# Optimization experiments

Hardware: AMD Instinct MI355X
Metric: run time of the kernel (lower is better)

## Reference

```python
import jax, jax.numpy as jnp
import numpy as np

B, N, D = 2, 128, 512  # batch, tokens, embed_dim (= in_features = out_features)
LAYERS = 3


def setup_inputs() -> dict:
    key = jax.random.key(0)
    ks = jax.random.split(key, 9)
    s = lambda fan_in: 1.0 / np.sqrt(fan_in)
    return {
        "text_embedding": jax.random.normal(ks[0], (B, N, D), dtype=jnp.float32),
        # weights stored as [in, out] so y = x @ W + b (matches torch Linear math)
        "W_rel": jax.random.uniform(ks[1], (2 * D, D), jnp.float32, -s(2 * D), s(2 * D)),
        "b_rel": jax.random.uniform(ks[2], (D,), jnp.float32, -s(2 * D), s(2 * D)),
        "W_go": jax.random.uniform(ks[3], (D, D), jnp.float32, -s(D), s(D)),
        "b_go": jax.random.uniform(ks[4], (D,), jnp.float32, -s(D), s(D)),
        "W_gr": jax.random.uniform(ks[5], (3 * D, D), jnp.float32, -s(3 * D), s(3 * D)),
        "b_gr": jax.random.uniform(ks[6], (D,), jnp.float32, -s(3 * D), s(3 * D)),
        "W_esa": jax.random.uniform(ks[7], (D, D), jnp.float32, -s(D), s(D)),
        "b_esa": jax.random.uniform(ks[8], (D,), jnp.float32, -s(D), s(D)),
    }


def reference(text_embedding, W_rel, b_rel, W_go, b_go, W_gr, b_gr, W_esa, b_esa):
    x = text_embedding  # [B, N, D]
    n = x.shape[1]
    rel = None
    for i in range(LAYERS):
        new_x = jnp.tanh(x @ W_go + b_go)  # [B, N, D]
        # pairwise broadcast-concat: [B, N, N, 2D]
        a = jnp.broadcast_to(x[:, :, None, :], (x.shape[0], n, n, x.shape[-1]))
        b = jnp.broadcast_to(x[:, None, :, :], (x.shape[0], n, n, x.shape[-1]))
        rlf = jnp.concatenate([a, b], axis=3)
        if i == 0:
            rel = rlf @ W_rel + b_rel  # [B, N, N, D]
        rlf2 = jnp.concatenate([rlf, rel], axis=3)  # [B, N, N, 3D]
        rel = jnp.tanh(rlf2 @ W_gr + b_gr)  # [B, N, N, D]
        x = new_x
    rel = rel @ W_esa + b_esa  # [B, N, N, D]
    # original subtracts max over dim=1 then applies Softmax(dim=1); equivalent to stable softmax over axis 1
    attn = jax.nn.softmax(rel, axis=1)
    rel_out = jnp.sum(attn * rel, axis=-2)  # sum over second N axis -> [B, N, D]
    return (x, rel_out)
```

## Files before the change

### kernel.cpp

```cpp
#include <hip/hip_runtime.h>
#include <hip/hip_bf16.h>
#include <stdint.h>


#define DEV static __device__ __forceinline__

typedef float  f32x4  __attribute__((ext_vector_type(4)));
typedef __bf16 bf16x8 __attribute__((ext_vector_type(8)));

DEV float tanh_fast(float x) {
  float e = __expf(2.0f * x);
  return 1.0f - __fdividef(2.0f, e + 1.0f);
}

DEV void gl_lds16(const void* g, void* l) {
  __builtin_amdgcn_global_load_lds(
      (const __attribute__((address_space(1))) unsigned int*)g,
      (__attribute__((address_space(3))) unsigned int*)l, 16, 0, 0);
}

__global__ __launch_bounds__(256) void wconv_kernel(
    const float* __restrict__ Wc, const float* __restrict__ We,
    __bf16* __restrict__ Wct, __bf16* __restrict__ Wet) {
  const float* W = blockIdx.y ? We : Wc;
  __bf16* Wt = blockIdx.y ? Wet : Wct;
  __shared__ float tile[32][33];
  int t = threadIdx.x;
  int tx = t & 31, ty = t >> 5;
  int bx = blockIdx.x & 15, by = blockIdx.x >> 4;
  int k0 = by * 32, n0 = bx * 32;
#pragma unroll
  for (int r = 0; r < 4; ++r) {
    int k = ty + r * 8;
    tile[k][tx] = W[(size_t)(k0 + k) * 512 + n0 + tx];
  }
  __syncthreads();
#pragma unroll
  for (int r = 0; r < 4; ++r) {
    int n = ty + r * 8;
    Wt[(size_t)(n0 + n) * 512 + k0 + tx] = (__bf16)tile[tx][n];
  }
}

struct SOp {
  const float* X;
  const float* W;
  const float* bias;
  const float* add;
  float* out;
  int M;
  int act;
};
struct SBatch { SOp op[6]; };

__global__ __launch_bounds__(256) void small_gemm_kernel(SBatch batch) {
  const SOp o = batch.op[blockIdx.y];
  const int r0 = (int)(blockIdx.x >> 3) * 16;
  const int c0 = (int)(blockIdx.x & 7) * 64;
  if (r0 >= o.M) return;
  __shared__ float Xs[16][40];
  __shared__ float Ws[32][64];
  const int t = threadIdx.x;
  const int tr = t >> 4;
  const int tc = (t & 15) * 4;
  float a0 = 0.f, a1 = 0.f, a2 = 0.f, a3 = 0.f;
  for (int k0 = 0; k0 < 512; k0 += 32) {
    __syncthreads();
    if (t < 128) {
      int row = t >> 3, col = (t & 7) * 4;
      float4 v = make_float4(0.f, 0.f, 0.f, 0.f);
      if (r0 + row < o.M) v = *(const float4*)&o.X[(size_t)(r0 + row) * 512 + k0 + col];
      *(float4*)&Xs[row][col] = v;
    }
    {
      int row = t >> 3, col = (t & 7) * 8;
      const float4* src = (const float4*)&o.W[(size_t)(k0 + row) * 512 + c0 + col];
      *(float4*)&Ws[row][col]     = src[0];
      *(float4*)&Ws[row][col + 4] = src[1];
    }
    __syncthreads();
#pragma unroll
    for (int k = 0; k < 32; ++k) {
      float a = Xs[tr][k];
      float4 w = *(float4*)&Ws[k][tc];
      a0 += a * w.x; a1 += a * w.y; a2 += a * w.z; a3 += a * w.w;
    }
  }
  const int row = r0 + tr;
  if (row >= o.M) return;
  float4 v = make_float4(a0, a1, a2, a3);
  if (o.bias) {
    float4 bv = *(const float4*)&o.bias[c0 + tc];
    v.x += bv.x; v.y += bv.y; v.z += bv.z; v.w += bv.w;
  }
  if (o.add) {
    float4 av = *(const float4*)&o.add[(size_t)row * 512 + c0 + tc];
    v.x += av.x; v.y += av.y; v.z += av.z; v.w += av.w;
  }
  if (o.act) { v.x = tanh_fast(v.x); v.y = tanh_fast(v.y); v.z = tanh_fast(v.z); v.w = tanh_fast(v.w); }
  *(float4*)&o.out[(size_t)row * 512 + c0 + tc] = v;
}

constexpr int BM = 128, BN = 128, BK = 64;

template <int MODE>
__global__ __launch_bounds__(256, 2) void big_gemm_kernel(
    const __bf16* __restrict__ Ab, const float* __restrict__ Av,
    const float* __restrict__ Cv, const __bf16* __restrict__ Wt,
    const float* __restrict__ P, const float* __restrict__ Q,
    const float* __restrict__ bias, __bf16* __restrict__ outb,
    float* __restrict__ outf) {
  __shared__ __bf16 As[BM * BK];
  __shared__ __bf16 Bs[BN * BK];
  const int t = threadIdx.x;
  const int lane = t & 63;
  const int wave = t >> 6;
  const int bm = (int)blockIdx.x >> 2;
  const int n0 = ((int)blockIdx.x & 3) * BN;
  const size_t r0 = (size_t)bm * BM;
  const int b = bm >> 7;
  const int i = bm & 127;
  const int waveM = wave >> 1, waveN = wave & 1;

  f32x4 vzero = {0.f, 0.f, 0.f, 0.f};
  f32x4 acc[4][4];
#pragma unroll
  for (int a = 0; a < 4; ++a)
#pragma unroll
    for (int c = 0; c < 4; ++c) acc[a][c] = vzero;

  const int jj = t >> 3;
  const int kc = (t & 7) * 8;

  for (int k0 = 0; k0 < 512; k0 += BK) {
    __syncthreads();
    if (MODE == 0) {
      float av[8];
      const float* ap = &Av[((size_t)(b * 128 + i)) * 512 + k0 + kc];
      *(float4*)&av[0] = *(const float4*)ap;
      *(float4*)&av[4] = *(const float4*)(ap + 4);
#pragma unroll
      for (int rnd = 0; rnd < 4; ++rnd) {
        int j = rnd * 32 + jj;
        const float* cp = &Cv[((size_t)(b * 128 + j)) * 512 + k0 + kc];
        float cv[8];
        *(float4*)&cv[0] = *(const float4*)cp;
        *(float4*)&cv[4] = *(const float4*)(cp + 4);
        bf16x8 o;
#pragma unroll
        for (int e = 0; e < 8; ++e) o[e] = (__bf16)tanh_fast(av[e] + cv[e]);
        *(bf16x8*)&As[j * BK + kc] = o;
      }
    } else {
#pragma unroll
      for (int p2 = 0; p2 < 4; ++p2) {
        int rowg = wave * 32 + p2 * 8;
        const __bf16* g = Ab + (r0 + rowg + (lane >> 3)) * 512 + k0 + (lane & 7) * 8;
        gl_lds16(g, &As[rowg * BK]);
      }
    }
#pragma unroll
    for (int p2 = 0; p2 < 4; ++p2) {
      int rowg = wave * 32 + p2 * 8;
      const __bf16* g = Wt + (size_t)(n0 + rowg + (lane >> 3)) * 512 + k0 + (lane & 7) * 8;
      gl_lds16(g, &Bs[rowg * BK]);
    }
    __syncthreads();
#pragma unroll
    for (int kk = 0; kk < 2; ++kk) {
      const int koff = kk * 32 + (lane >> 4) * 8;
      const int ml = lane & 15;
      bf16x8 af[4], bfr[4];
#pragma unroll
      for (int tm = 0; tm < 4; ++tm)
        af[tm] = *(const bf16x8*)&As[(waveM * 64 + tm * 16 + ml) * BK + koff];
#pragma unroll
      for (int tn = 0; tn < 4; ++tn)
        bfr[tn] = *(const bf16x8*)&Bs[(waveN * 64 + tn * 16 + ml) * BK + koff];
#pragma unroll
      for (int tm = 0; tm < 4; ++tm)
#pragma unroll
        for (int tn = 0; tn < 4; ++tn)
          acc[tm][tn] = __builtin_amdgcn_mfma_f32_16x16x32_bf16(af[tm], bfr[tn], acc[tm][tn], 0, 0, 0);
    }
  }

  const int quad = lane >> 4, cl = lane & 15;
#pragma unroll
  for (int tm = 0; tm < 4; ++tm) {
#pragma unroll
    for (int r = 0; r < 4; ++r) {
      const int row = waveM * 64 + tm * 16 + quad * 4 + r;
      const size_t grow = r0 + row;
#pragma unroll
      for (int tn = 0; tn < 4; ++tn) {
        const int col = n0 + waveN * 64 + tn * 16 + cl;
        float v = acc[tm][tn][r];
        if (MODE == 2) {
          v += bias[col];
          outf[grow * 512 + col] = v;
        } else {
          v += P[((size_t)(b * 128 + i)) * 512 + col] +
               Q[((size_t)(b * 128 + row)) * 512 + col];
          outb[grow * 512 + col] = (__bf16)tanh_fast(v);
        }
      }
    }
  }
}

__global__ __launch_bounds__(256) void softmax_ml_kernel(
    const float* __restrict__ S, float* __restrict__ Mb, float* __restrict__ Lb) {
  int idx = blockIdx.x * 256 + threadIdx.x;
  int d = idx & 511;
  int j = (idx >> 9) & 127;
  int b = idx >> 16;
  const float* p = S + ((size_t)b * 16384 + j) * 512 + d;
  float m = -3.4e38f, l = 0.f;
  for (int ii = 0; ii < 128; ++ii) {
    float s = p[(size_t)ii * 65536];
    float nm = fmaxf(m, s);
    l = l * __expf(m - nm) + __expf(s - nm);
    m = nm;
  }
  Mb[idx] = m;
  Lb[idx] = 1.0f / l;
}

__global__ __launch_bounds__(256) void softmax_out_kernel(
    const float* __restrict__ S, const float* __restrict__ Mb,
    const float* __restrict__ Lb, float* __restrict__ outp) {
  int idx = blockIdx.x * 256 + threadIdx.x;
  int d = idx & 511;
  int i = (idx >> 9) & 127;
  int b = idx >> 16;
  const float* sp = S + ((size_t)(b * 128 + i)) * 65536 + d;
  const float* mp = Mb + (size_t)b * 65536 + d;
  const float* lp = Lb + (size_t)b * 65536 + d;
  float acc = 0.f;
  for (int jj = 0; jj < 128; ++jj) {
    float s = sp[(size_t)jj * 512];
    float w = __expf(s - mp[(size_t)jj * 512]) * lp[(size_t)jj * 512];
    acc += w * s;
  }
  outp[idx] = acc;
}

extern "C" void kernel_launch(void* const* d_in, const int* in_sizes, int n_in,
                              void* d_out, int out_size, void* d_ws, size_t ws_size,
                              hipStream_t stream) {
  const float* x0    = (const float*)d_in[0];
  const float* W_rel = (const float*)d_in[1];
  const float* b_rel = (const float*)d_in[2];
  const float* W_go  = (const float*)d_in[3];
  const float* b_go  = (const float*)d_in[4];
  const float* W_gr  = (const float*)d_in[5];
  const float* b_gr  = (const float*)d_in[6];
  const float* W_esa = (const float*)d_in[7];
  const float* b_esa = (const float*)d_in[8];

  const float* Wrel_top = W_rel;
  const float* Wrel_bot = W_rel + 512 * 512;
  const float* Wgr_a = W_gr;
  const float* Wgr_b = W_gr + 512 * 512;
  const float* Wgr_c = W_gr + 2 * 512 * 512;

  char* ws = (char*)d_ws;
  size_t off = 0;
  auto alloc = [&](size_t bytes) -> void* {
    void* p = ws + off;
    off += (bytes + 255) & ~(size_t)255;
    return p;
  };
  const size_t NREL = 16777216ull;
  float*  S     = (float*)alloc(NREL * 4);
  __bf16* relA  = (__bf16*)alloc(NREL * 2);
  __bf16* relB  = (__bf16*)alloc(NREL * 2);
  float* x1  = (float*)alloc(131072 * 4);
  float* x2  = (float*)alloc(131072 * 4);
  float* u0  = (float*)alloc(131072 * 4);
  float* v0  = (float*)alloc(131072 * 4);
  float* p0t = (float*)alloc(131072 * 4);
  float* q0t = (float*)alloc(131072 * 4);
  float* Abuf = (float*)alloc(131072 * 4);
  float* Cbuf = (float*)alloc(131072 * 4);
  float* p1  = (float*)alloc(131072 * 4);
  float* q1  = (float*)alloc(131072 * 4);
  float* p2  = (float*)alloc(131072 * 4);
  float* q2  = (float*)alloc(131072 * 4);
  float* dvec = (float*)alloc(512 * 4);
  float* Mb  = (float*)alloc(131072 * 4);
  float* Lb  = (float*)alloc(131072 * 4);
  __bf16* Wg3t  = (__bf16*)alloc(262144 * 2);
  __bf16* Wesat = (__bf16*)alloc(262144 * 2);

  float* x3out  = (float*)d_out;
  float* relout = (float*)d_out + 131072;

  wconv_kernel<<<dim3(256, 2), 256, 0, stream>>>(Wgr_c, W_esa, Wg3t, Wesat);

  SBatch b1 = {};
  b1.op[0] = {x0, W_go, b_go, nullptr, x1, 256, 1};
  b1.op[1] = {x0, Wrel_top, nullptr, nullptr, u0, 256, 0};
  b1.op[2] = {x0, Wrel_bot, nullptr, nullptr, v0, 256, 0};
  b1.op[3] = {x0, Wgr_a, nullptr, nullptr, p0t, 256, 0};
  b1.op[4] = {x0, Wgr_b, nullptr, nullptr, q0t, 256, 0};
  b1.op[5] = {b_rel, Wgr_c, b_gr, nullptr, dvec, 1, 0};
  small_gemm_kernel<<<dim3(128, 6), 256, 0, stream>>>(b1);

  SBatch b2 = {};
  b2.op[0] = {x1, W_go, b_go, nullptr, x2, 256, 1};
  b2.op[1] = {u0, Wgr_c, dvec, p0t, Abuf, 256, 0};
  b2.op[2] = {v0, Wgr_c, nullptr, q0t, Cbuf, 256, 0};
  b2.op[3] = {x1, Wgr_a, b_gr, nullptr, p1, 256, 0};
  b2.op[4] = {x1, Wgr_b, nullptr, nullptr, q1, 256, 0};
  small_gemm_kernel<<<dim3(128, 5), 256, 0, stream>>>(b2);

  SBatch b3 = {};
  b3.op[0] = {x2, W_go, b_go, nullptr, x3out, 256, 1};
  b3.op[1] = {x2, Wgr_a, b_gr, nullptr, p2, 256, 0};
  b3.op[2] = {x2, Wgr_b, nullptr, nullptr, q2, 256, 0};
  small_gemm_kernel<<<dim3(128, 3), 256, 0, stream>>>(b3);

  big_gemm_kernel<0><<<1024, 256, 0, stream>>>(nullptr, Abuf, Cbuf, Wg3t, p1, q1,
                                               nullptr, relA, nullptr);
  big_gemm_kernel<1><<<1024, 256, 0, stream>>>(relA, nullptr, nullptr, Wg3t, p2, q2,
                                               nullptr, relB, nullptr);
  big_gemm_kernel<2><<<1024, 256, 0, stream>>>(relB, nullptr, nullptr, Wesat, nullptr,
                                               nullptr, b_esa, nullptr, S);

  softmax_ml_kernel<<<512, 256, 0, stream>>>(S, Mb, Lb);
  softmax_out_kernel<<<512, 256, 0, stream>>>(S, Mb, Lb, relout);
}
```

Before: 283.5 us.

## Move small GEMMs to split-bf16 MFMA and materialize first rel layer separately

The small fp32 SIMT GEMMs are replaced with an MFMA kernel that uses a hi/lo bf16 split (three MFMAs per tile) to keep near-fp32 accuracy. Weights and activations are pre-split into hi/lo bf16 buffers, and dvec gets its own tiny kernel. The tanh(A+C) expansion that fed the first big GEMM now runs in a separate elementwise kernel that writes a 32MB bf16 buffer, so every big GEMM can use the direct global-to-LDS load path. This adds extra launches and an extra full-tensor write and read of the first rel layer in exchange for faster small GEMMs.

```diff
diff --git a/kernel.cpp b/kernel.cpp
--- a/kernel.cpp
+++ b/kernel.cpp
@@ -7,6 +7,7 @@
 
 typedef float  f32x4  __attribute__((ext_vector_type(4)));
 typedef __bf16 bf16x8 __attribute__((ext_vector_type(8)));
+typedef __bf16 bf16x4 __attribute__((ext_vector_type(4)));
 
 DEV float tanh_fast(float x) {
   float e = __expf(2.0f * x);
@@ -19,11 +20,11 @@
       (__attribute__((address_space(3))) unsigned int*)l, 16, 0, 0);
 }
 
-__global__ __launch_bounds__(256) void wconv_kernel(
-    const float* __restrict__ Wc, const float* __restrict__ We,
-    __bf16* __restrict__ Wct, __bf16* __restrict__ Wet) {
-  const float* W = blockIdx.y ? We : Wc;
-  __bf16* Wt = blockIdx.y ? Wet : Wct;
+struct WC { const float* W; __bf16* Wh; __bf16* Wl; };
+struct WCBatch { WC w[7]; };
+
+__global__ __launch_bounds__(256) void wconv_kernel(WCBatch wb) {
+  const WC wc = wb.w[blockIdx.y];
   __shared__ float tile[32][33];
   int t = threadIdx.x;
   int tx = t & 31, ty = t >> 5;
@@ -32,81 +33,169 @@
 #pragma unroll
   for (int r = 0; r < 4; ++r) {
     int k = ty + r * 8;
-    tile[k][tx] = W[(size_t)(k0 + k) * 512 + n0 + tx];
+    tile[k][tx] = wc.W[(size_t)(k0 + k) * 512 + n0 + tx];
   }
   __syncthreads();
 #pragma unroll
   for (int r = 0; r < 4; ++r) {
     int n = ty + r * 8;
-    Wt[(size_t)(n0 + n) * 512 + k0 + tx] = (__bf16)tile[tx][n];
-  }
-}
-
-struct SOp {
-  const float* X;
-  const float* W;
+    float v = tile[tx][n];
+    __bf16 h = (__bf16)v;
+    wc.Wh[(size_t)(n0 + n) * 512 + k0 + tx] = h;
+    wc.Wl[(size_t)(n0 + n) * 512 + k0 + tx] = (__bf16)(v - (float)h);
+  }
+}
+
+__global__ __launch_bounds__(256) void xconv_kernel(
+    const float* __restrict__ x, __bf16* __restrict__ xh, __bf16* __restrict__ xl) {
+  int i = blockIdx.x * 256 + threadIdx.x;
+  float4 v = ((const float4*)x)[i];
+  float vv[4] = {v.x, v.y, v.z, v.w};
+  bf16x4 h, l;
+#pragma unroll
+  for (int e = 0; e < 4; ++e) {
+    __bf16 he = (__bf16)vv[e];
+    h[e] = he;
+    l[e] = (__bf16)(vv[e] - (float)he);
+  }
+  ((bf16x4*)xh)[i] = h;
+  ((bf16x4*)xl)[i] = l;
+}
+
+__global__ __launch_bounds__(256) void dvec_kernel(
+    const float* __restrict__ b_rel, const float* __restrict__ Wgrc,
+    const float* __restrict__ b_gr, float* __restrict__ dvec) {
+  int n = blockIdx.x * 256 + threadIdx.x;
+  float acc = b_gr[n];
+#pragma unroll 8
+  for (int k = 0; k < 512; ++k) acc += b_rel[k] * Wgrc[(size_t)k * 512 + n];
+  dvec[n] = acc;
+}
+
+struct MOp {
+  const __bf16* Xh; const __bf16* Xl;
+  const __bf16* Wh; const __bf16* Wl;
   const float* bias;
   const float* add;
-  float* out;
-  int M;
+  float* outf;
+  __bf16* outh; __bf16* outl;
   int act;
 };
-struct SBatch { SOp op[6]; };
-
-__global__ __launch_bounds__(256) void small_gemm_kernel(SBatch batch) {
-  const SOp o = batch.op[blockIdx.y];
-  const int r0 = (int)(blockIdx.x >> 3) * 16;
-  const int c0 = (int)(blockIdx.x & 7) * 64;
-  if (r0 >= o.M) return;
-  __shared__ float Xs[16][40];
-  __shared__ float Ws[32][64];
-  const int t = threadIdx.x;
-  const int tr = t >> 4;
-  const int tc = (t & 15) * 4;
-  float a0 = 0.f, a1 = 0.f, a2 = 0.f, a3 = 0.f;
-  for (int k0 = 0; k0 < 512; k0 += 32) {
+struct MBatch { MOp op[5]; };
+
+__global__ __launch_bounds__(256, 2) void mfma_small_kernel(MBatch batch) {
+  const MOp o = batch.op[blockIdx.y];
+  const int m0 = ((int)blockIdx.x >> 3) * 64;
+  const int n0 = ((int)blockIdx.x & 7) * 64;
+  __shared__ __bf16 Ah[64 * 64], Al[64 * 64], Bh[64 * 64], Bl[64 * 64];
+  const int t = threadIdx.x, lane = t & 63, wave = t >> 6;
+  const int waveM = wave >> 1, waveN = wave & 1;
+  const bool comp = (o.Xl != nullptr);
+
+  f32x4 vzero = {0.f, 0.f, 0.f, 0.f};
+  f32x4 acc[2][2];
+#pragma unroll
+  for (int a = 0; a < 2; ++a)
+#pragma unroll
+    for (int c = 0; c < 2; ++c) acc[a][c] = vzero;
+
+  const int lr = lane >> 3, lc = (lane & 7) * 8;
+
+  for (int k0 = 0; k0 < 512; k0 += 64) {
     __syncthreads();
-    if (t < 128) {
-      int row = t >> 3, col = (t & 7) * 4;
-      float4 v = make_float4(0.f, 0.f, 0.f, 0.f);
-      if (r0 + row < o.M) v = *(const float4*)&o.X[(size_t)(r0 + row) * 512 + k0 + col];
-      *(float4*)&Xs[row][col] = v;
-    }
-    {
-      int row = t >> 3, col = (t & 7) * 8;
-      const float4* src = (const float4*)&o.W[(size_t)(k0 + row) * 512 + c0 + col];
-      *(float4*)&Ws[row][col]     = src[0];
-      *(float4*)&Ws[row][col + 4] = src[1];
+#pragma unroll
+    for (int r = 0; r < 2; ++r) {
+      const int rb = r * 32 + wave * 8;
+      gl_lds16(o.Xh + (size_t)(m0 + rb + lr) * 512 + k0 + lc, &Ah[rb * 64]);
+      gl_lds16(o.Wh + (size_t)(n0 + rb + lr) * 512 + k0 + lc, &Bh[rb * 64]);
+      if (comp) {
+        gl_lds16(o.Xl + (size_t)(m0 + rb + lr) * 512 + k0 + lc, &Al[rb * 64]);
+        gl_lds16(o.Wl + (size_t)(n0 + rb + lr) * 512 + k0 + lc, &Bl[rb * 64]);
+      }
     }
     __syncthreads();
 #pragma unroll
-    for (int k = 0; k < 32; ++k) {
-      float a = Xs[tr][k];
-      float4 w = *(float4*)&Ws[k][tc];
-      a0 += a * w.x; a1 += a * w.y; a2 += a * w.z; a3 += a * w.w;
-    }
-  }
-  const int row = r0 + tr;
-  if (row >= o.M) return;
-  float4 v = make_float4(a0, a1, a2, a3);
-  if (o.bias) {
-    float4 bv = *(const float4*)&o.bias[c0 + tc];
-    v.x += bv.x; v.y += bv.y; v.z += bv.z; v.w += bv.w;
-  }
-  if (o.add) {
-    float4 av = *(const float4*)&o.add[(size_t)row * 512 + c0 + tc];
-    v.x += av.x; v.y += av.y; v.z += av.z; v.w += av.w;
-  }
-  if (o.act) { v.x = tanh_fast(v.x); v.y = tanh_fast(v.y); v.z = tanh_fast(v.z); v.w = tanh_fast(v.w); }
-  *(float4*)&o.out[(size_t)row * 512 + c0 + tc] = v;
+    for (int kk = 0; kk < 2; ++kk) {
+      const int koff = kk * 32 + (lane >> 4) * 8;
+      const int ml = lane & 15;
+      bf16x8 ah[2], bh[2], al[2], bl[2];
+#pragma unroll
+      for (int tm = 0; tm < 2; ++tm)
+        ah[tm] = *(const bf16x8*)&Ah[(waveM * 32 + tm * 16 + ml) * 64 + koff];
+#pragma unroll
+      for (int tn = 0; tn < 2; ++tn)
+        bh[tn] = *(const bf16x8*)&Bh[(waveN * 32 + tn * 16 + ml) * 64 + koff];
+      if (comp) {
+#pragma unroll
+        for (int tm = 0; tm < 2; ++tm)
+          al[tm] = *(const bf16x8*)&Al[(waveM * 32 + tm * 16 + ml) * 64 + koff];
+#pragma unroll
+        for (int tn = 0; tn < 2; ++tn)
+          bl[tn] = *(const bf16x8*)&Bl[(waveN * 32 + tn * 16 + ml) * 64 + koff];
+      }
+#pragma unroll
+      for (int tm = 0; tm < 2; ++tm)
+#pragma unroll
+        for (int tn = 0; tn < 2; ++tn) {
+          acc[tm][tn] = __builtin_amdgcn_mfma_f32_16x16x32_bf16(ah[tm], bh[tn], acc[tm][tn], 0, 0, 0);
+          if (comp) {
+            acc[tm][tn] = __builtin_amdgcn_mfma_f32_16x16x32_bf16(ah[tm], bl[tn], acc[tm][tn], 0, 0, 0);
+            acc[tm][tn] = __builtin_amdgcn_mfma_f32_16x16x32_bf16(al[tm], bh[tn], acc[tm][tn], 0, 0, 0);
+          }
+        }
+    }
+  }
+
+  const int quad = lane >> 4, cl = lane & 15;
+#pragma unroll
+  for (int tm = 0; tm < 2; ++tm) {
+#pragma unroll
+    for (int r = 0; r < 4; ++r) {
+      const int row = m0 + waveM * 32 + tm * 16 + quad * 4 + r;
+#pragma unroll
+      for (int tn = 0; tn < 2; ++tn) {
+        const int col = n0 + waveN * 32 + tn * 16 + cl;
+        float v = acc[tm][tn][r];
+        if (o.bias) v += o.bias[col];
+        if (o.add) v += o.add[(size_t)row * 512 + col];
+        if (o.act) v = tanh_fast(v);
+        if (o.outf) o.outf[(size_t)row * 512 + col] = v;
+        if (o.outh) {
+          __bf16 h = (__bf16)v;
+          o.outh[(size_t)row * 512 + col] = h;
+          o.outl[(size_t)row * 512 + col] = (__bf16)(v - (float)h);
+        }
+      }
+    }
+  }
+}
+
+__global__ __launch_bounds__(256) void rel1_kernel(
+    const float* __restrict__ A, const float* __restrict__ C,
+    __bf16* __restrict__ R1) {
+  size_t e = ((size_t)blockIdx.x * 256 + threadIdx.x) * 8;
+  int d = (int)(e & 511);
+  int j = (int)((e >> 9) & 127);
+  int bi = (int)(e >> 16);
+  int b = bi >> 7;
+  const float* ap = &A[(size_t)bi * 512 + d];
+  const float* cp = &C[((size_t)(b * 128 + j)) * 512 + d];
+  float av[8], cv[8];
+  *(float4*)&av[0] = *(const float4*)ap;
+  *(float4*)&av[4] = *(const float4*)(ap + 4);
+  *(float4*)&cv[0] = *(const float4*)cp;
+  *(float4*)&cv[4] = *(const float4*)(cp + 4);
+  bf16x8 o;
+#pragma unroll
+  for (int k = 0; k < 8; ++k) o[k] = (__bf16)tanh_fast(av[k] + cv[k]);
+  *(bf16x8*)&R1[e] = o;
 }
 
 constexpr int BM = 128, BN = 128, BK = 64;
 
 template <int MODE>
 __global__ __launch_bounds__(256, 2) void big_gemm_kernel(
-    const __bf16* __restrict__ Ab, const float* __restrict__ Av,
-    const float* __restrict__ Cv, const __bf16* __restrict__ Wt,
+    const __bf16* __restrict__ Ab, const __bf16* __restrict__ Wt,
     const float* __restrict__ P, const float* __restrict__ Q,
     const float* __restrict__ bias, __bf16* __restrict__ outb,
     float* __restrict__ outf) {
@@ -129,41 +218,15 @@
 #pragma unroll
     for (int c = 0; c < 4; ++c) acc[a][c] = vzero;
 
-  const int jj = t >> 3;
-  const int kc = (t & 7) * 8;
-
   for (int k0 = 0; k0 < 512; k0 += BK) {
     __syncthreads();
-    if (MODE == 0) {
-      float av[8];
-      const float* ap = &Av[((size_t)(b * 128 + i)) * 512 + k0 + kc];
-      *(float4*)&av[0] = *(const float4*)ap;
-      *(float4*)&av[4] = *(const float4*)(ap + 4);
-#pragma unroll
-      for (int rnd = 0; rnd < 4; ++rnd) {
-        int j = rnd * 32 + jj;
-        const float* cp = &Cv[((size_t)(b * 128 + j)) * 512 + k0 + kc];
-        float cv[8];
-        *(float4*)&cv[0] = *(const float4*)cp;
-        *(float4*)&cv[4] = *(const float4*)(cp + 4);
-        bf16x8 o;
-#pragma unroll
-        for (int e = 0; e < 8; ++e) o[e] = (__bf16)tanh_fast(av[e] + cv[e]);
-        *(bf16x8*)&As[j * BK + kc] = o;
-      }
-    } else {
-#pragma unroll
-      for (int p2 = 0; p2 < 4; ++p2) {
-        int rowg = wave * 32 + p2 * 8;
-        const __bf16* g = Ab + (r0 + rowg + (lane >> 3)) * 512 + k0 + (lane & 7) * 8;
-        gl_lds16(g, &As[rowg * BK]);
-      }
-    }
 #pragma unroll
     for (int p2 = 0; p2 < 4; ++p2) {
       int rowg = wave * 32 + p2 * 8;
-      const __bf16* g = Wt + (size_t)(n0 + rowg + (lane >> 3)) * 512 + k0 + (lane & 7) * 8;
-      gl_lds16(g, &Bs[rowg * BK]);
+      const __bf16* ga = Ab + (r0 + rowg + (lane >> 3)) * 512 + k0 + (lane & 7) * 8;
+      gl_lds16(ga, &As[rowg * BK]);
+      const __bf16* gb = Wt + (size_t)(n0 + rowg + (lane >> 3)) * 512 + k0 + (lane & 7) * 8;
+      gl_lds16(gb, &Bs[rowg * BK]);
     }
     __syncthreads();
 #pragma unroll
@@ -273,61 +336,87 @@
     return p;
   };
   const size_t NREL = 16777216ull;
-  float*  S     = (float*)alloc(NREL * 4);
-  __bf16* relA  = (__bf16*)alloc(NREL * 2);
-  __bf16* relB  = (__bf16*)alloc(NREL * 2);
-  float* x1  = (float*)alloc(131072 * 4);
-  float* x2  = (float*)alloc(131072 * 4);
-  float* u0  = (float*)alloc(131072 * 4);
-  float* v0  = (float*)alloc(131072 * 4);
-  float* p0t = (float*)alloc(131072 * 4);
-  float* q0t = (float*)alloc(131072 * 4);
+  float*  S  = (float*)alloc(NREL * 4);
+  __bf16* R1 = (__bf16*)alloc(NREL * 2);
+  __bf16* R2 = (__bf16*)alloc(NREL * 2);
+  float* p0t  = (float*)alloc(131072 * 4);
+  float* q0t  = (float*)alloc(131072 * 4);
   float* Abuf = (float*)alloc(131072 * 4);
   float* Cbuf = (float*)alloc(131072 * 4);
-  float* p1  = (float*)alloc(131072 * 4);
-  float* q1  = (float*)alloc(131072 * 4);
-  float* p2  = (float*)alloc(131072 * 4);
-  float* q2  = (float*)alloc(131072 * 4);
+  float* p1   = (float*)alloc(131072 * 4);
+  float* q1   = (float*)alloc(131072 * 4);
+  float* p2   = (float*)alloc(131072 * 4);
+  float* q2   = (float*)alloc(131072 * 4);
   float* dvec = (float*)alloc(512 * 4);
-  float* Mb  = (float*)alloc(131072 * 4);
-  float* Lb  = (float*)alloc(131072 * 4);
-  __bf16* Wg3t  = (__bf16*)alloc(262144 * 2);
-  __bf16* Wesat = (__bf16*)alloc(262144 * 2);
+  float* Mb   = (float*)alloc(131072 * 4);
+  float* Lb   = (float*)alloc(131072 * 4);
+  __bf16* x0h = (__bf16*)alloc(131072 * 2);
+  __bf16* x0l = (__bf16*)alloc(131072 * 2);
+  __bf16* x1h = (__bf16*)alloc(131072 * 2);
+  __bf16* x1l = (__bf16*)alloc(131072 * 2);
+  __bf16* x2h = (__bf16*)alloc(131072 * 2);
+  __bf16* x2l = (__bf16*)alloc(131072 * 2);
+  __bf16* u0h = (__bf16*)alloc(131072 * 2);
+  __bf16* u0l = (__bf16*)alloc(131072 * 2);
+  __bf16* v0h = (__bf16*)alloc(131072 * 2);
+  __bf16* v0l = (__bf16*)alloc(131072 * 2);
+  __bf16* Wgo_h = (__bf16*)alloc(262144 * 2);
+  __bf16* Wgo_l = (__bf16*)alloc(262144 * 2);
+  __bf16* Wrt_h = (__bf16*)alloc(262144 * 2);
+  __bf16* Wrt_l = (__bf16*)alloc(262144 * 2);
+  __bf16* Wrb_h = (__bf16*)alloc(262144 * 2);
+  __bf16* Wrb_l = (__bf16*)alloc(262144 * 2);
+  __bf16* Wga_h = (__bf16*)alloc(262144 * 2);
+  __bf16* Wga_l = (__bf16*)alloc(262144 * 2);
+  __bf16* Wgb_h = (__bf16*)alloc(262144 * 2);
+  __bf16* Wgb_l = (__bf16*)alloc(262144 * 2);
+  __bf16* Wgc_h = (__bf16*)alloc(262144 * 2);
+  __bf16* Wgc_l = (__bf16*)alloc(262144 * 2);
+  __bf16* Wes_h = (__bf16*)alloc(262144 * 2);
+  __bf16* Wes_l = (__bf16*)alloc(262144 * 2);
 
   float* x3out  = (float*)d_out;
   float* relout = (float*)d_out + 131072;
 
-  wconv_kernel<<<dim3(256, 2), 256, 0, stream>>>(Wgr_c, W_esa, Wg3t, Wesat);
-
-  SBatch b1 = {};
-  b1.op[0] = {x0, W_go, b_go, nullptr, x1, 256, 1};
-  b1.op[1] = {x0, Wrel_top, nullptr, nullptr, u0, 256, 0};
-  b1.op[2] = {x0, Wrel_bot, nullptr, nullptr, v0, 256, 0};
-  b1.op[3] = {x0, Wgr_a, nullptr, nullptr, p0t, 256, 0};
-  b1.op[4] = {x0, Wgr_b, nullptr, nullptr, q0t, 256, 0};
-  b1.op[5] = {b_rel, Wgr_c, b_gr, nullptr, dvec, 1, 0};
-  small_gemm_kernel<<<dim3(128, 6), 256, 0, stream>>>(b1);
-
-  SBatch b2 = {};
-  b2.op[0] = {x1, W_go, b_go, nullptr, x2, 256, 1};
-  b2.op[1] = {u0, Wgr_c, dvec, p0t, Abuf, 256, 0};
-  b2.op[2] = {v0, Wgr_c, nullptr, q0t, Cbuf, 256, 0};
-  b2.op[3] = {x1, Wgr_a, b_gr, nullptr, p1, 256, 0};
-  b2.op[4] = {x1, Wgr_b, nullptr, nullptr, q1, 256, 0};
-  small_gemm_kernel<<<dim3(128, 5), 256, 0, stream>>>(b2);
-
-  SBatch b3 = {};
-  b3.op[0] = {x2, W_go, b_go, nullptr, x3out, 256, 1};
-  b3.op[1] = {x2, Wgr_a, b_gr, nullptr, p2, 256, 0};
-  b3.op[2] = {x2, Wgr_b, nullptr, nullptr, q2, 256, 0};
-  small_gemm_kernel<<<dim3(128, 3), 256, 0, stream>>>(b3);
-
-  big_gemm_kernel<0><<<1024, 256, 0, stream>>>(nullptr, Abuf, Cbuf, Wg3t, p1, q1,
-                                               nullptr, relA, nullptr);
-  big_gemm_kernel<1><<<1024, 256, 0, stream>>>(relA, nullptr, nullptr, Wg3t, p2, q2,
-                                               nullptr, relB, nullptr);
-  big_gemm_kernel<2><<<1024, 256, 0, stream>>>(relB, nullptr, nullptr, Wesat, nullptr,
-                                               nullptr, b_esa, nullptr, S);
+  WCBatch wb;
+  wb.w[0] = {W_go, Wgo_h, Wgo_l};
+  wb.w[1] = {Wrel_top, Wrt_h, Wrt_l};
+  wb.w[2] = {Wrel_bot, Wrb_h, Wrb_l};
+  wb.w[3] = {Wgr_a, Wga_h, Wga_l};
+  wb.w[4] = {Wgr_b, Wgb_h, Wgb_l};
+  wb.w[5] = {Wgr_c, Wgc_h, Wgc_l};
+  wb.w[6] = {W_esa, Wes_h, Wes_l};
+  wconv_kernel<<<dim3(256, 7), 256, 0, stream>>>(wb);
+  xconv_kernel<<<128, 256, 0, stream>>>(x0, x0h, x0l);
+  dvec_kernel<<<2, 256, 0, stream>>>(b_rel, Wgr_c, b_gr, dvec);
+
+  MBatch m1 = {};
+  m1.op[0] = {x0h, x0l, Wgo_h, Wgo_l, b_go, nullptr, nullptr, x1h, x1l, 1};
+  m1.op[1] = {x0h, x0l, Wrt_h, Wrt_l, nullptr, nullptr, nullptr, u0h, u0l, 0};
+  m1.op[2] = {x0h, x0l, Wrb_h, Wrb_l, nullptr, nullptr, nullptr, v0h, v0l, 0};
+  m1.op[3] = {x0h, x0l, Wga_h, Wga_l, nullptr, nullptr, p0t, nullptr, nullptr, 0};
+  m1.op[4] = {x0h, x0l, Wgb_h, Wgb_l, nullptr, nullptr, q0t, nullptr, nullptr, 0};
+  mfma_small_kernel<<<dim3(32, 5), 256, 0, stream>>>(m1);
+
+  MBatch m2 = {};
+  m2.op[0] = {x1h, x1l, Wgo_h, Wgo_l, b_go, nullptr, nullptr, x2h, x2l, 1};
+  m2.op[1] = {u0h, u0l, Wgc_h, Wgc_l, dvec, p0t, Abuf, nullptr, nullptr, 0};
+  m2.op[2] = {v0h, v0l, Wgc_h, Wgc_l, nullptr, q0t, Cbuf, nullptr, nullptr, 0};
+  m2.op[3] = {x1h, x1l, Wga_h, Wga_l, b_gr, nullptr, p1, nullptr, nullptr, 0};
+  m2.op[4] = {x1h, x1l, Wgb_h, Wgb_l, nullptr, nullptr, q1, nullptr, nullptr, 0};
+  mfma_small_kernel<<<dim3(32, 5), 256, 0, stream>>>(m2);
+
+  MBatch m3 = {};
+  m3.op[0] = {x2h, x2l, Wgo_h, Wgo_l, b_go, nullptr, x3out, nullptr, nullptr, 1};
+  m3.op[1] = {x2h, x2l, Wga_h, Wga_l, b_gr, nullptr, p2, nullptr, nullptr, 0};
+  m3.op[2] = {x2h, x2l, Wgb_h, Wgb_l, nullptr, nullptr, q2, nullptr, nullptr, 0};
+  mfma_small_kernel<<<dim3(32, 3), 256, 0, stream>>>(m3);
+
+  rel1_kernel<<<8192, 256, 0, stream>>>(Abuf, Cbuf, R1);
+
+  big_gemm_kernel<1><<<1024, 256, 0, stream>>>(R1, Wgc_h, p1, q1, nullptr, R2, nullptr);
+  big_gemm_kernel<1><<<1024, 256, 0, stream>>>(R2, Wgc_h, p2, q2, nullptr, R1, nullptr);
+  big_gemm_kernel<2><<<1024, 256, 0, stream>>>(R1, Wes_h, nullptr, nullptr, b_esa, nullptr, S);
 
   softmax_ml_kernel<<<512, 256, 0, stream>>>(S, Mb, Lb);
   softmax_out_kernel<<<512, 256, 0, stream>>>(S, Mb, Lb, relout);
```

Result: faster. 277.4 us (-2.1%).
